# Optimization experiments

Measured on AMD Instinct MI355X. Metric: run time of the kernel, lower is better.

## Reference

```python
import jax, jax.numpy as jnp
import numpy as np

EMB = 1024
HEADS = 16
S = EMB // HEADS  # 64
B, T = 2, 2048


def setup_inputs() -> dict:
    key = jax.random.key(0)
    ks = jax.random.split(key, 5)
    x = jax.random.normal(ks[0], (B, T, EMB), dtype=jnp.float32)
    Wk = jax.random.normal(ks[1], (S, S), dtype=jnp.float32) * (1.0 / np.sqrt(S))
    Wq = jax.random.normal(ks[2], (S, S), dtype=jnp.float32) * (1.0 / np.sqrt(S))
    Wv = jax.random.normal(ks[3], (S, S), dtype=jnp.float32) * (1.0 / np.sqrt(S))
    Wu = jax.random.normal(ks[4], (EMB, EMB), dtype=jnp.float32) * (1.0 / np.sqrt(EMB))
    bu = jnp.zeros((EMB,), dtype=jnp.float32)
    return {"x": x, "Wk": Wk, "Wq": Wq, "Wv": Wv, "Wu": Wu, "bu": bu}


def reference(x, Wk, Wq, Wv, Wu, bu):
    b, t, e = x.shape
    h, s = HEADS, e // HEADS
    xh = x.reshape(b, t, h, s)
    # torch Linear: y = x @ W.T (per-head projection, weights shared across heads)
    keys = jnp.einsum('bths,os->btho', xh, Wk)
    queries = jnp.einsum('bths,os->btho', xh, Wq)
    values = jnp.einsum('bths,os->btho', xh, Wv)
    scale = e ** (-0.25)
    queries = queries * scale
    keys = keys * scale
    # [b, h, t_q, t_k] full score matrix (as in the original bmm)
    dot = jnp.einsum('bqhd,bkhd->bhqk', queries, keys)
    attn = jax.nn.softmax(dot, axis=-1)
    out = jnp.einsum('bhqk,bkhd->bqhd', attn, values).reshape(b, t, e)
    return out @ Wu.T + bu
```

## Files before the change

### kernel.cpp

```cpp
#include <hip/hip_runtime.h>
#include <hip/hip_bf16.h>
#include <stdint.h>

#define TT   2048
#define EMB  1024
#define SDIM 64
#define KVB  128
#define NIT  (TT / KVB)
#define LOG2E 1.4426950408889634f

typedef float f32x2  __attribute__((ext_vector_type(2)));
typedef float f32x4  __attribute__((ext_vector_type(4)));
typedef float f32x16 __attribute__((ext_vector_type(16)));
typedef short short8 __attribute__((ext_vector_type(8)));
typedef unsigned short ushort4v __attribute__((ext_vector_type(4)));
typedef unsigned int uint2v __attribute__((ext_vector_type(2)));
typedef unsigned int uint4v __attribute__((ext_vector_type(4)));

__device__ __forceinline__ ushort f2bf(float f) {
    uint32_t u = __builtin_bit_cast(uint32_t, f);
    u += 0x7FFFu + ((u >> 16) & 1u);
    return (ushort)(u >> 16);
}

__device__ __forceinline__ short8 cvt8(const float* p) {
    f32x4 a = *(const f32x4*)p;
    f32x4 b = *(const f32x4*)(p + 4);
    short8 r;
    r[0] = (short)f2bf(a[0]); r[1] = (short)f2bf(a[1]);
    r[2] = (short)f2bf(a[2]); r[3] = (short)f2bf(a[3]);
    r[4] = (short)f2bf(b[0]); r[5] = (short)f2bf(b[1]);
    r[6] = (short)f2bf(b[2]); r[7] = (short)f2bf(b[3]);
    return r;
}

__device__ __forceinline__ void gload16(const void* g, void* l) {
    __builtin_amdgcn_global_load_lds((const __attribute__((address_space(1))) uint32_t*)g,
                                     (__attribute__((address_space(3))) uint32_t*)l, 16, 0, 0);
}
__device__ __forceinline__ uint pkbf(float a, float b) {
    uint d; asm("v_cvt_pk_bf16_f32 %0, %1, %2" : "=v"(d) : "v"(a), "v"(b)); return d;
}
__device__ __forceinline__ void swap32(uint& a, uint& b) {
    asm volatile("s_nop 1\n\tv_permlane32_swap_b32 %0, %1" : "+v"(a), "+v"(b));
}
__device__ __forceinline__ float xhadd(float x) {
    uint a = __builtin_bit_cast(uint, x), o;
    asm volatile("v_mov_b32 %0, %1\n\ts_nop 3\n\tv_permlane32_swap_b32 %0, %1"
                 : "=&v"(o), "+v"(a));
    return __builtin_bit_cast(float, o) + __builtin_bit_cast(float, a);
}

__global__ __launch_bounds__(256) void cvt_w(const float* __restrict__ Wk, const float* __restrict__ Wq,
                                             const float* __restrict__ Wv,
                                             ushort* __restrict__ Wk16, ushort* __restrict__ Wq16,
                                             ushort* __restrict__ Wv16) {
    int i = blockIdx.x * 256 + threadIdx.x;
    Wk16[i] = f2bf(Wk[i]);
    Wq16[i] = f2bf(Wq[i] * (0.03125f * LOG2E));
    Wv16[i] = f2bf(Wv[i]);
}

__global__ __launch_bounds__(256) void qkv(const float* __restrict__ x,
                                           const ushort* __restrict__ Wk16, const ushort* __restrict__ Wq16,
                                           const ushort* __restrict__ Wv16,
                                           ushort* __restrict__ Qw, ushort* __restrict__ Kw, ushort* __restrict__ Vt,
                                           const float* __restrict__ Wu, ushort* __restrict__ Wu16) {
    const int tid = threadIdx.x;
    if (blockIdx.x >= 1024) {
        const int gbase = ((blockIdx.x - 1024) * 256 + tid) * 16;
#pragma unroll
        for (int j = 0; j < 4; ++j) {
            f32x4 v = *(const f32x4*)(Wu + gbase + 4 * j);
            ushort4v o;
#pragma unroll
            for (int e = 0; e < 4; ++e) o[e] = f2bf(v[e]);
            *(ushort4v*)(Wu16 + gbase + 4 * j) = o;
        }
        return;
    }
    const int wave = tid >> 6, lane = tid & 63;
    const int c = lane & 15, g = lane >> 4;
    const int rblk = (blockIdx.x * 4 + wave) * 16;
    const int bh = rblk >> 11;
    const int tbase = rblk & (TT - 1);
    const int b = bh >> 4, h = bh & 15;

    const float* xrow = x + ((size_t)(b * TT + tbase + c) * EMB + h * SDIM);
    short8 a[2];
#pragma unroll
    for (int ks = 0; ks < 2; ++ks) a[ks] = cvt8(xrow + 32 * ks + 8 * g);

    f32x4 aq[4], ak[4], av[4];
#pragma unroll
    for (int n = 0; n < 4; ++n) { aq[n] = 0.f; ak[n] = 0.f; av[n] = 0.f; }

#pragma unroll
    for (int n = 0; n < 4; ++n) {
#pragma unroll
        for (int ks = 0; ks < 2; ++ks) {
            const size_t wo = (size_t)(16 * n + c) * SDIM + 32 * ks + 8 * g;
            short8 bq = *(const short8*)(Wq16 + wo);
            short8 bk = *(const short8*)(Wk16 + wo);
            short8 bv = *(const short8*)(Wv16 + wo);
            aq[n] = __builtin_amdgcn_mfma_f32_16x16x32_bf16(a[ks], bq, aq[n], 0, 0, 0);
            ak[n] = __builtin_amdgcn_mfma_f32_16x16x32_bf16(a[ks], bk, ak[n], 0, 0, 0);
            av[n] = __builtin_amdgcn_mfma_f32_16x16x32_bf16(a[ks], bv, av[n], 0, 0, 0);
        }
    }
    const size_t hb = (size_t)bh * TT * SDIM;
#pragma unroll
    for (int n = 0; n < 4; ++n) {
#pragma unroll
        for (int i = 0; i < 4; ++i) {
            const size_t o = hb + (size_t)(tbase + 4 * g + i) * SDIM + 16 * n + c;
            Qw[o] = f2bf(aq[n][i]);
            Kw[o] = f2bf(ak[n][i]);
        }
        ushort4v vp;
#pragma unroll
        for (int i = 0; i < 4; ++i) vp[i] = f2bf(av[n][i]);
        *(ushort4v*)(Vt + hb + (size_t)(16 * n + c) * TT + tbase + 4 * g) = vp;
    }
}

__global__ __launch_bounds__(512, 4) void attn(const ushort* __restrict__ Qw, const ushort* __restrict__ Kw,
                                               const ushort* __restrict__ Vt, ushort* __restrict__ AO) {
    __shared__ ushort smem[4][8192];

    const int tid = threadIdx.x;
    const int wv = tid >> 6, lane = tid & 63;
    const int q = lane & 31, hi = lane >> 5;
    const int qg = wv & 3, kh = wv >> 2;
    const int wo = kh * 64;

    const int wg = blockIdx.x;
    const int xcd = wg & 7, slot = wg >> 3;
    const int bh = xcd * 4 + (slot >> 4);
    const int qt = slot & 15;
    const int b = bh >> 4, h = bh & 15;
    const int qrowW = qt * 128 + qg * 32;
    const size_t base = (size_t)bh * TT * SDIM;

    short8 qa[4];
    const ushort* Qp = Qw + base + (size_t)(qrowW + q) * SDIM + 8 * hi;
#pragma unroll
    for (int sb = 0; sb < 4; ++sb) qa[sb] = *(const short8*)(Qp + 16 * sb);

    f32x16 a0v = 0.f, a1v = 0.f;
    float lsum = 0.f;

    const int krow = lane >> 3;
    const ushort* Ks = Kw + base + (size_t)(wv * 8 + krow) * SDIM + (((lane & 7) ^ krow) * 8);
    const int vrow = wv * 4 + (lane >> 4);
    const ushort* Vs = Vt + base + (size_t)vrow * TT + (((lane & 15) ^ (vrow & 15)) * 8);

#define STAGE(kvb, buf) { \
    char* kb = (char*)&smem[(buf)][0] + wv * 1024;      \
    char* vb = (char*)&smem[2 + (buf)][0] + wv * 1024;  \
    _Pragma("unroll")                                    \
    for (int p = 0; p < 2; ++p) {                        \
        gload16(Ks + (kvb) * 64 + p * 4096, kb + p * 8192); \
        gload16(Vs + (kvb) + p * 32 * TT,   vb + p * 8192); \
    } }

    STAGE(0, 0);
    __syncthreads();

    const int kmask = (q & 7) << 4;
    const int vmask = q & 15;
    int cur = 0;
    for (int kt = 0; kt < NIT; ++kt) {
        if (kt < NIT - 1) STAGE((kt + 1) * KVB, cur ^ 1);
        const char* Kc = (const char*)&smem[cur][0];
        const char* Vc = (const char*)&smem[2 + cur][0];

        f32x16 s0 = 0.f, s1 = 0.f;
#pragma unroll
        for (int sb = 0; sb < 4; ++sb) {
            const int off = (32 * sb + 16 * hi) ^ kmask;
            short8 k0 = *(const short8*)(Kc + (wo + q) * 128 + off);
            s0 = __builtin_amdgcn_mfma_f32_32x32x16_bf16(k0, qa[sb], s0, 0, 0, 0);
            short8 k1 = *(const short8*)(Kc + (wo + 32 + q) * 128 + off);
            s1 = __builtin_amdgcn_mfma_f32_32x32x16_bf16(k1, qa[sb], s1, 0, 0, 0);
        }

        float r0 = 0.f, r1 = 0.f;
#pragma unroll
        for (int i = 0; i < 16; ++i) { float p = __builtin_amdgcn_exp2f(s0[i]); s0[i] = p; r0 += p; }
#pragma unroll
        for (int i = 0; i < 16; ++i) { float p = __builtin_amdgcn_exp2f(s1[i]); s1[i] = p; r1 += p; }
        lsum += r0 + r1;

        short8 pb0, pb1, pb2, pb3;
#define RP(sv, pa_, pb_) { \
        uint u0 = pkbf(sv[0], sv[1]),   u1 = pkbf(sv[2], sv[3]);   \
        uint u2 = pkbf(sv[4], sv[5]),   u3 = pkbf(sv[6], sv[7]);   \
        swap32(u0, u2); swap32(u1, u3);                            \
        uint4v ta = {u0, u1, u2, u3}; pa_ = __builtin_bit_cast(short8, ta); \
        uint u4 = pkbf(sv[8], sv[9]),   u5 = pkbf(sv[10], sv[11]); \
        uint u6 = pkbf(sv[12], sv[13]), u7 = pkbf(sv[14], sv[15]); \
        swap32(u4, u6); swap32(u5, u7);                            \
        uint4v tb = {u4, u5, u6, u7}; pb_ = __builtin_bit_cast(short8, tb); }
        RP(s0, pb0, pb1) RP(s1, pb2, pb3)
#undef RP

#define PV(kstep, pbk) { \
        const int u = ((2 * (kstep) + hi + kh * 8) ^ vmask) << 4;          \
        short8 v0 = *(const short8*)(Vc + q * 256 + u);                    \
        a0v = __builtin_amdgcn_mfma_f32_32x32x16_bf16(v0, pbk, a0v, 0, 0, 0); \
        short8 v1 = *(const short8*)(Vc + (32 + q) * 256 + u);             \
        a1v = __builtin_amdgcn_mfma_f32_32x32x16_bf16(v1, pbk, a1v, 0, 0, 0); }
        PV(0, pb0) PV(1, pb1) PV(2, pb2) PV(3, pb3)
#undef PV

        __syncthreads();
        cur ^= 1;
    }
#undef STAGE

    f32x2* ob = (f32x2*)&smem[0][0];
    float* lb = (float*)&smem[0][0] + 8192;
    const int mb = qg * 1024 + lane;
    if (kh) {
#pragma unroll
        for (int j = 0; j < 8; ++j) { f32x2 t = {a0v[2 * j], a0v[2 * j + 1]}; ob[mb + j * 64] = t; }
#pragma unroll
        for (int j = 0; j < 8; ++j) { f32x2 t = {a1v[2 * j], a1v[2 * j + 1]}; ob[mb + (8 + j) * 64] = t; }
        lb[qg * 64 + lane] = lsum;
    }
    __syncthreads();
    if (kh) return;

#pragma unroll
    for (int j = 0; j < 8; ++j) { f32x2 t = ob[mb + j * 64];       a0v[2 * j] += t[0]; a0v[2 * j + 1] += t[1]; }
#pragma unroll
    for (int j = 0; j < 8; ++j) { f32x2 t = ob[mb + (8 + j) * 64]; a1v[2 * j] += t[0]; a1v[2 * j + 1] += t[1]; }
    lsum += lb[qg * 64 + lane];

    const float l_i = xhadd(lsum);
    char* scrB = (char*)&smem[0][0] + 40960 + qg * 4096;
    const int eswz = (q & 7) << 4;
    float inv = 1.f / l_i;
#pragma unroll
    for (int sb2 = 0; sb2 < 2; ++sb2) {
#pragma unroll
        for (int bq = 0; bq < 4; ++bq) {
            float v0 = (sb2 ? a1v[4 * bq + 0] : a0v[4 * bq + 0]) * inv;
            float v1 = (sb2 ? a1v[4 * bq + 1] : a0v[4 * bq + 1]) * inv;
            float v2 = (sb2 ? a1v[4 * bq + 2] : a0v[4 * bq + 2]) * inv;
            float v3 = (sb2 ? a1v[4 * bq + 3] : a0v[4 * bq + 3]) * inv;
            uint2v d; d[0] = pkbf(v0, v1); d[1] = pkbf(v2, v3);
            int s0e = 8 * bq + 4 * hi + 32 * sb2;
            *(uint2v*)(scrB + q * 128 + ((s0e * 2) ^ eswz)) = d;
        }
    }
    asm volatile("s_waitcnt lgkmcnt(0)" ::: "memory");
    ushort* AOp = AO + (size_t)(b * TT + qrowW + q) * EMB + h * SDIM + 32 * hi;
#pragma unroll
    for (int jj = 0; jj < 4; ++jj) {
        short8 o = *(const short8*)(scrB + q * 128 + ((64 * hi + 16 * jj) ^ eswz));
        *(short8*)(AOp + 8 * jj) = o;
    }
}

__global__ __launch_bounds__(512) void oproj(const ushort* __restrict__ AO, const ushort* __restrict__ Wu16,
                                             const float* __restrict__ bu, float* __restrict__ out) {
    __shared__ ushort Ab[2][128 * 64];
    __shared__ ushort Bb[2][128 * 64];
    const int tid = threadIdx.x;
    const int wv = tid >> 6, lane = tid & 63;
    const int c = lane & 15, g = lane >> 4;
    const int wr = wv >> 1, wc = wv & 1;
    const int wg = blockIdx.x;
    const int xcd = wg & 7, i6 = wg >> 3;
    const int rblk = (xcd * 4 + (i6 >> 3)) * 128;
    const int nblk = (i6 & 7) * 128;

    const int row0 = tid >> 3;
    const int col0 = ((tid & 7) ^ (row0 & 7)) * 8;
    const ushort* As0 = AO   + (size_t)(rblk + row0) * EMB + col0;
    const ushort* As1 = AO   + (size_t)(rblk + row0 + 64) * EMB + col0;
    const ushort* Bs0 = Wu16 + (size_t)(nblk + row0) * EMB + col0;
    const ushort* Bs1 = Wu16 + (size_t)(nblk + row0 + 64) * EMB + col0;
    const int l0 = wv * 512, l1 = 4096 + wv * 512;

    f32x4 acc[2][4];
#pragma unroll
    for (int m = 0; m < 2; ++m)
#pragma unroll
        for (int n = 0; n < 4; ++n) acc[m][n] = 0.f;

    gload16(As0, &Ab[0][l0]); gload16(As1, &Ab[0][l1]);
    gload16(Bs0, &Bb[0][l0]); gload16(Bs1, &Bb[0][l1]);
    __syncthreads();

    const int swzA = (c & 7) << 4;
    int cur = 0;
    for (int kt = 0; kt < 16; ++kt) {
        if (kt < 15) {
            const int k0 = (kt + 1) * 64;
            gload16(As0 + k0, &Ab[cur ^ 1][l0]); gload16(As1 + k0, &Ab[cur ^ 1][l1]);
            gload16(Bs0 + k0, &Bb[cur ^ 1][l0]); gload16(Bs1 + k0, &Bb[cur ^ 1][l1]);
        }
        const char* Ac = (const char*)&Ab[cur][0];
        const char* Bc = (const char*)&Bb[cur][0];
#pragma unroll
        for (int kb = 0; kb < 2; ++kb) {
            short8 am[2], bn[4];
#pragma unroll
            for (int m = 0; m < 2; ++m)
                am[m] = *(const short8*)(Ac + (wr * 32 + 16 * m + c) * 128 + ((64 * kb + 16 * g) ^ swzA));
#pragma unroll
            for (int n = 0; n < 4; ++n)
                bn[n] = *(const short8*)(Bc + (wc * 64 + 16 * n + c) * 128 + ((64 * kb + 16 * g) ^ swzA));
#pragma unroll
            for (int m = 0; m < 2; ++m)
#pragma unroll
                for (int n = 0; n < 4; ++n)
                    acc[m][n] = __builtin_amdgcn_mfma_f32_16x16x32_bf16(am[m], bn[n], acc[m][n], 0, 0, 0);
        }
        __syncthreads();
        cur ^= 1;
    }
#pragma unroll
    for (int m = 0; m < 2; ++m)
#pragma unroll
        for (int n = 0; n < 4; ++n) {
            float bias = bu[nblk + wc * 64 + 16 * n + c];
#pragma unroll
            for (int i = 0; i < 4; ++i)
                out[(size_t)(rblk + wr * 32 + 16 * m + 4 * g + i) * EMB + nblk + wc * 64 + 16 * n + c] =
                    acc[m][n][i] + bias;
        }
}

extern "C" void kernel_launch(void* const* d_in, const int* in_sizes, int n_in,
                              void* d_out, int out_size, void* d_ws, size_t ws_size,
                              hipStream_t stream) {
    const float* x  = (const float*)d_in[0];
    const float* Wk = (const float*)d_in[1];
    const float* Wq = (const float*)d_in[2];
    const float* Wv = (const float*)d_in[3];
    const float* Wu = (const float*)d_in[4];
    const float* bu = (const float*)d_in[5];
    float* out = (float*)d_out;

    char* ws = (char*)d_ws;
    const size_t MB = 1024u * 1024u;
    ushort* Qw   = (ushort*)(ws);
    ushort* Kw   = (ushort*)(ws + 8 * MB);
    ushort* Vt   = (ushort*)(ws + 16 * MB);
    ushort* AO   = (ushort*)(ws + 24 * MB);
    ushort* Wu16 = (ushort*)(ws + 32 * MB);
    ushort* Wk16 = (ushort*)(ws + 34 * MB);
    ushort* Wq16 = Wk16 + 4096;
    ushort* Wv16 = Wk16 + 8192;

    cvt_w<<<dim3(16), dim3(256), 0, stream>>>(Wk, Wq, Wv, Wk16, Wq16, Wv16);
    qkv<<<dim3(1280), dim3(256), 0, stream>>>(x, Wk16, Wq16, Wv16, Qw, Kw, Vt, Wu, Wu16);
    attn<<<dim3(512), dim3(512), 0, stream>>>(Qw, Kw, Vt, AO);
    oproj<<<dim3(256), dim3(512), 0, stream>>>(AO, Wu16, bu, out);
}
```

Measured before the change: 84.79 us.

## Shrink attention workgroups to 64 query rows and 64-key tiles

Attention blocks shrink from 512 threads covering 128 query rows with 128-key tiles to 256 threads covering 64 query rows with 64-key tiles, doubling the grid to 1024 workgroups and halving LDS use. Each wave now handles one 32-key half per tile, which cuts registers and should improve occupancy and load balance across CUs. s_setprio is also raised around the MFMA sections to favour matrix issue. The trade-off is twice as many loop iterations and barriers per workgroup, and more total K/V loads from global memory.

```diff
diff --git a/kernel.cpp b/kernel.cpp
--- a/kernel.cpp
+++ b/kernel.cpp
@@ -5,7 +5,7 @@
 #define TT   2048
 #define EMB  1024
 #define SDIM 64
-#define KVB  128
+#define KVB  64
 #define NIT  (TT / KVB)
 #define LOG2E 1.4426950408889634f
 
@@ -124,22 +124,21 @@
     }
 }
 
-__global__ __launch_bounds__(512, 4) void attn(const ushort* __restrict__ Qw, const ushort* __restrict__ Kw,
+__global__ __launch_bounds__(256, 4) void attn(const ushort* __restrict__ Qw, const ushort* __restrict__ Kw,
                                                const ushort* __restrict__ Vt, ushort* __restrict__ AO) {
-    __shared__ ushort smem[4][8192];
+    __shared__ ushort smem[4][4096];
 
     const int tid = threadIdx.x;
     const int wv = tid >> 6, lane = tid & 63;
     const int q = lane & 31, hi = lane >> 5;
-    const int qg = wv & 3, kh = wv >> 2;
-    const int wo = kh * 64;
+    const int qg = wv & 1, kh = wv >> 1;
 
     const int wg = blockIdx.x;
     const int xcd = wg & 7, slot = wg >> 3;
-    const int bh = xcd * 4 + (slot >> 4);
-    const int qt = slot & 15;
+    const int bh = xcd * 4 + (slot >> 5);
+    const int qt = slot & 31;
     const int b = bh >> 4, h = bh & 15;
-    const int qrowW = qt * 128 + qg * 32;
+    const int qrowW = qt * 64 + qg * 32;
     const size_t base = (size_t)bh * TT * SDIM;
 
     short8 qa[4];
@@ -151,68 +150,67 @@
     float lsum = 0.f;
 
     const int krow = lane >> 3;
-    const ushort* Ks = Kw + base + (size_t)(wv * 8 + krow) * SDIM + (((lane & 7) ^ krow) * 8);
-    const int vrow = wv * 4 + (lane >> 4);
-    const ushort* Vs = Vt + base + (size_t)vrow * TT + (((lane & 15) ^ (vrow & 15)) * 8);
+    const ushort* Ks = Kw + base + (size_t)(wv * 8 + krow) * SDIM + (((lane & 7) ^ (krow & 7)) * 8);
+    const ushort* Vs = Vt + base + (size_t)(wv * 8 + krow) * TT + (((lane & 7) ^ (krow & 7)) * 8);
 
 #define STAGE(kvb, buf) { \
     char* kb = (char*)&smem[(buf)][0] + wv * 1024;      \
     char* vb = (char*)&smem[2 + (buf)][0] + wv * 1024;  \
     _Pragma("unroll")                                    \
     for (int p = 0; p < 2; ++p) {                        \
-        gload16(Ks + (kvb) * 64 + p * 4096, kb + p * 8192); \
-        gload16(Vs + (kvb) + p * 32 * TT,   vb + p * 8192); \
+        gload16(Ks + (kvb) * 64 + p * 2048, kb + p * 4096); \
+        gload16(Vs + (kvb) + p * 32 * TT,   vb + p * 4096); \
     } }
 
     STAGE(0, 0);
     __syncthreads();
 
     const int kmask = (q & 7) << 4;
-    const int vmask = q & 15;
+    const int vmask = q & 7;
     int cur = 0;
     for (int kt = 0; kt < NIT; ++kt) {
         if (kt < NIT - 1) STAGE((kt + 1) * KVB, cur ^ 1);
         const char* Kc = (const char*)&smem[cur][0];
         const char* Vc = (const char*)&smem[2 + cur][0];
 
-        f32x16 s0 = 0.f, s1 = 0.f;
+        f32x16 s0 = 0.f;
+        __builtin_amdgcn_s_setprio(1);
 #pragma unroll
         for (int sb = 0; sb < 4; ++sb) {
             const int off = (32 * sb + 16 * hi) ^ kmask;
-            short8 k0 = *(const short8*)(Kc + (wo + q) * 128 + off);
+            short8 k0 = *(const short8*)(Kc + (kh * 32 + q) * 128 + off);
             s0 = __builtin_amdgcn_mfma_f32_32x32x16_bf16(k0, qa[sb], s0, 0, 0, 0);
-            short8 k1 = *(const short8*)(Kc + (wo + 32 + q) * 128 + off);
-            s1 = __builtin_amdgcn_mfma_f32_32x32x16_bf16(k1, qa[sb], s1, 0, 0, 0);
-        }
-
-        float r0 = 0.f, r1 = 0.f;
+        }
+        __builtin_amdgcn_s_setprio(0);
+
+        float r0 = 0.f;
 #pragma unroll
         for (int i = 0; i < 16; ++i) { float p = __builtin_amdgcn_exp2f(s0[i]); s0[i] = p; r0 += p; }
-#pragma unroll
-        for (int i = 0; i < 16; ++i) { float p = __builtin_amdgcn_exp2f(s1[i]); s1[i] = p; r1 += p; }
-        lsum += r0 + r1;
-
-        short8 pb0, pb1, pb2, pb3;
-#define RP(sv, pa_, pb_) { \
-        uint u0 = pkbf(sv[0], sv[1]),   u1 = pkbf(sv[2], sv[3]);   \
-        uint u2 = pkbf(sv[4], sv[5]),   u3 = pkbf(sv[6], sv[7]);   \
-        swap32(u0, u2); swap32(u1, u3);                            \
-        uint4v ta = {u0, u1, u2, u3}; pa_ = __builtin_bit_cast(short8, ta); \
-        uint u4 = pkbf(sv[8], sv[9]),   u5 = pkbf(sv[10], sv[11]); \
-        uint u6 = pkbf(sv[12], sv[13]), u7 = pkbf(sv[14], sv[15]); \
-        swap32(u4, u6); swap32(u5, u7);                            \
-        uint4v tb = {u4, u5, u6, u7}; pb_ = __builtin_bit_cast(short8, tb); }
-        RP(s0, pb0, pb1) RP(s1, pb2, pb3)
-#undef RP
-
-#define PV(kstep, pbk) { \
-        const int u = ((2 * (kstep) + hi + kh * 8) ^ vmask) << 4;          \
-        short8 v0 = *(const short8*)(Vc + q * 256 + u);                    \
-        a0v = __builtin_amdgcn_mfma_f32_32x32x16_bf16(v0, pbk, a0v, 0, 0, 0); \
-        short8 v1 = *(const short8*)(Vc + (32 + q) * 256 + u);             \
-        a1v = __builtin_amdgcn_mfma_f32_32x32x16_bf16(v1, pbk, a1v, 0, 0, 0); }
-        PV(0, pb0) PV(1, pb1) PV(2, pb2) PV(3, pb3)
-#undef PV
+        lsum += r0;
+
+        short8 pb0, pb1;
+        {
+            uint u0 = pkbf(s0[0], s0[1]),   u1 = pkbf(s0[2], s0[3]);
+            uint u2 = pkbf(s0[4], s0[5]),   u3 = pkbf(s0[6], s0[7]);
+            swap32(u0, u2); swap32(u1, u3);
+            uint4v ta = {u0, u1, u2, u3}; pb0 = __builtin_bit_cast(short8, ta);
+            uint u4 = pkbf(s0[8], s0[9]),   u5 = pkbf(s0[10], s0[11]);
+            uint u6 = pkbf(s0[12], s0[13]), u7 = pkbf(s0[14], s0[15]);
+            swap32(u4, u6); swap32(u5, u7);
+            uint4v tb = {u4, u5, u6, u7}; pb1 = __builtin_bit_cast(short8, tb);
+        }
+
+        __builtin_amdgcn_s_setprio(1);
+#pragma unroll
+        for (int ks = 0; ks < 2; ++ks) {
+            short8 pbk = ks ? pb1 : pb0;
+            const int u = ((4 * kh + 2 * ks + hi) ^ vmask) << 4;
+            short8 v0 = *(const short8*)(Vc + q * 128 + u);
+            a0v = __builtin_amdgcn_mfma_f32_32x32x16_bf16(v0, pbk, a0v, 0, 0, 0);
+            short8 v1 = *(const short8*)(Vc + (32 + q) * 128 + u);
+            a1v = __builtin_amdgcn_mfma_f32_32x32x16_bf16(v1, pbk, a1v, 0, 0, 0);
+        }
+        __builtin_amdgcn_s_setprio(0);
 
         __syncthreads();
         cur ^= 1;
@@ -220,7 +218,7 @@
 #undef STAGE
 
     f32x2* ob = (f32x2*)&smem[0][0];
-    float* lb = (float*)&smem[0][0] + 8192;
+    float* lb = (float*)&smem[0][0] + 4096;
     const int mb = qg * 1024 + lane;
     if (kh) {
 #pragma unroll
@@ -239,7 +237,7 @@
     lsum += lb[qg * 64 + lane];
 
     const float l_i = xhadd(lsum);
-    char* scrB = (char*)&smem[0][0] + 40960 + qg * 4096;
+    char* scrB = (char*)&smem[0][0] + 20480 + qg * 4096;
     const int eswz = (q & 7) << 4;
     float inv = 1.f / l_i;
 #pragma unroll
@@ -359,6 +357,6 @@
 
     cvt_w<<<dim3(16), dim3(256), 0, stream>>>(Wk, Wq, Wv, Wk16, Wq16, Wv16);
     qkv<<<dim3(1280), dim3(256), 0, stream>>>(x, Wk16, Wq16, Wv16, Qw, Kw, Vt, Wu, Wu16);
-    attn<<<dim3(512), dim3(512), 0, stream>>>(Qw, Kw, Vt, AO);
+    attn<<<dim3(1024), dim3(256), 0, stream>>>(Qw, Kw, Vt, AO);
     oproj<<<dim3(256), dim3(512), 0, stream>>>(AO, Wu16, bu, out);
 }
```

Measured after the change: 88.80 us. 4.7% more time.

## Read V directly from global memory instead of staging through LDS

Applied to the files above, without the earlier changes.

Drops the LDS staging of the transposed V tile and has each wave load its V fragments for the PV MFMA straight from global memory (served by L2/L1). This halves shared memory per block (from 64KB to 34KB), which can raise occupancy and removes LDS write/read traffic for V. The cost is that V global loads now sit on the critical path inside the loop without software prefetch, and the epilogue gains an extra barrier so the output scratch can reuse the freed LDS region.

```diff
diff --git a/kernel.cpp b/kernel.cpp
--- a/kernel.cpp
+++ b/kernel.cpp
@@ -126,7 +126,7 @@
 
 __global__ __launch_bounds__(512, 4) void attn(const ushort* __restrict__ Qw, const ushort* __restrict__ Kw,
                                                const ushort* __restrict__ Vt, ushort* __restrict__ AO) {
-    __shared__ ushort smem[4][8192];
+    __shared__ ushort smem[17408];
 
     const int tid = threadIdx.x;
     const int wv = tid >> 6, lane = tid & 63;
@@ -152,28 +152,24 @@
 
     const int krow = lane >> 3;
     const ushort* Ks = Kw + base + (size_t)(wv * 8 + krow) * SDIM + (((lane & 7) ^ krow) * 8);
-    const int vrow = wv * 4 + (lane >> 4);
-    const ushort* Vs = Vt + base + (size_t)vrow * TT + (((lane & 15) ^ (vrow & 15)) * 8);
+    const ushort* Vp0 = Vt + base + (size_t)q * TT;
+    const ushort* Vp1 = Vt + base + (size_t)(32 + q) * TT;
 
 #define STAGE(kvb, buf) { \
-    char* kb = (char*)&smem[(buf)][0] + wv * 1024;      \
-    char* vb = (char*)&smem[2 + (buf)][0] + wv * 1024;  \
+    char* kb = (char*)smem + (buf) * 16384 + wv * 1024;  \
     _Pragma("unroll")                                    \
-    for (int p = 0; p < 2; ++p) {                        \
-        gload16(Ks + (kvb) * 64 + p * 4096, kb + p * 8192); \
-        gload16(Vs + (kvb) + p * 32 * TT,   vb + p * 8192); \
-    } }
+    for (int p = 0; p < 2; ++p)                          \
+        gload16(Ks + (size_t)(kvb) * 64 + p * 4096, kb + p * 8192); }
 
     STAGE(0, 0);
     __syncthreads();
 
     const int kmask = (q & 7) << 4;
-    const int vmask = q & 15;
     int cur = 0;
     for (int kt = 0; kt < NIT; ++kt) {
-        if (kt < NIT - 1) STAGE((kt + 1) * KVB, cur ^ 1);
-        const char* Kc = (const char*)&smem[cur][0];
-        const char* Vc = (const char*)&smem[2 + cur][0];
+        const int kvb = kt * KVB;
+        if (kt < NIT - 1) STAGE(kvb + KVB, cur ^ 1);
+        const char* Kc = (const char*)smem + cur * 16384;
 
         f32x16 s0 = 0.f, s1 = 0.f;
 #pragma unroll
@@ -206,10 +202,10 @@
 #undef RP
 
 #define PV(kstep, pbk) { \
-        const int u = ((2 * (kstep) + hi + kh * 8) ^ vmask) << 4;          \
-        short8 v0 = *(const short8*)(Vc + q * 256 + u);                    \
+        const int tcol = kvb + (2 * (kstep) + hi + 8 * kh) * 8;            \
+        short8 v0 = *(const short8*)(Vp0 + tcol);                          \
         a0v = __builtin_amdgcn_mfma_f32_32x32x16_bf16(v0, pbk, a0v, 0, 0, 0); \
-        short8 v1 = *(const short8*)(Vc + (32 + q) * 256 + u);             \
+        short8 v1 = *(const short8*)(Vp1 + tcol);                          \
         a1v = __builtin_amdgcn_mfma_f32_32x32x16_bf16(v1, pbk, a1v, 0, 0, 0); }
         PV(0, pb0) PV(1, pb1) PV(2, pb2) PV(3, pb3)
 #undef PV
@@ -219,8 +215,8 @@
     }
 #undef STAGE
 
-    f32x2* ob = (f32x2*)&smem[0][0];
-    float* lb = (float*)&smem[0][0] + 8192;
+    f32x2* ob = (f32x2*)smem;
+    float* lb = (float*)((char*)smem + 32768);
     const int mb = qg * 1024 + lane;
     if (kh) {
 #pragma unroll
@@ -230,16 +226,18 @@
         lb[qg * 64 + lane] = lsum;
     }
     __syncthreads();
+    if (!kh) {
+#pragma unroll
+        for (int j = 0; j < 8; ++j) { f32x2 t = ob[mb + j * 64];       a0v[2 * j] += t[0]; a0v[2 * j + 1] += t[1]; }
+#pragma unroll
+        for (int j = 0; j < 8; ++j) { f32x2 t = ob[mb + (8 + j) * 64]; a1v[2 * j] += t[0]; a1v[2 * j + 1] += t[1]; }
+        lsum += lb[qg * 64 + lane];
+    }
+    __syncthreads();
     if (kh) return;
 
-#pragma unroll
-    for (int j = 0; j < 8; ++j) { f32x2 t = ob[mb + j * 64];       a0v[2 * j] += t[0]; a0v[2 * j + 1] += t[1]; }
-#pragma unroll
-    for (int j = 0; j < 8; ++j) { f32x2 t = ob[mb + (8 + j) * 64]; a1v[2 * j] += t[0]; a1v[2 * j + 1] += t[1]; }
-    lsum += lb[qg * 64 + lane];
-
     const float l_i = xhadd(lsum);
-    char* scrB = (char*)&smem[0][0] + 40960 + qg * 4096;
+    char* scrB = (char*)smem + qg * 4096;
     const int eswz = (q & 7) << 4;
     float inv = 1.f / l_i;
 #pragma unroll
```

Result: slower. 118.2 us (+39.5%).
